# Optimization experiments

Measured on AMD Instinct MI355X. Metric: run time of the kernel, lower is better.

## Reference

```python
import jax, jax.numpy as jnp
import numpy as np

N = 100000   # nodes
E = 1600000  # edges
G = 512      # graphs
ATOM = 64
HID = 64
CLS = 10


def layer_norm(x, g, b, eps=1e-5):
    mu = jnp.mean(x, axis=-1, keepdims=True)
    var = jnp.mean((x - mu) ** 2, axis=-1, keepdims=True)
    return (x - mu) * jax.lax.rsqrt(var + eps) * g + b


def gcn_conv(x, src, dst, W, b, fill, num_nodes):
    # PyG GCNConv with add_self_loops: A_hat = A + fill*I, sym-normalized.
    h = x @ W                                            # [N, F_out]
    ones = jnp.ones(src.shape[0], dtype=h.dtype)
    deg = jax.ops.segment_sum(ones, dst, num_segments=num_nodes) + fill
    dinv = jax.lax.rsqrt(deg)                            # deg^{-1/2}
    norm = dinv[src] * dinv[dst]                         # [E]
    msg = h[src] * norm[:, None]                         # gather + scale
    out = jax.ops.segment_sum(msg, dst, num_segments=num_nodes)
    out = out + (fill * dinv * dinv)[:, None] * h        # self-loop term
    return out + b


def setup_inputs() -> dict:
    key = jax.random.key(0)
    ks = jax.random.split(key, 8)
    x = jax.random.normal(ks[0], (N, ATOM), dtype=jnp.float32)
    edge_index = jax.random.randint(ks[1], (2, E), 0, N, dtype=jnp.int64)
    batch = jnp.sort(jax.random.randint(ks[2], (N,), 0, G, dtype=jnp.int64))
    s = lambda k, sh, fan: jax.random.normal(k, sh, jnp.float32) / np.sqrt(fan)
    return {
        "x": x, "edge_index": edge_index, "batch": batch,
        "W1": s(ks[3], (ATOM, HID), ATOM), "b1": jnp.zeros((HID,), jnp.float32),
        "ln_g": jnp.ones((HID,), jnp.float32), "ln_b": jnp.zeros((HID,), jnp.float32),
        "W2": s(ks[4], (HID, HID), HID), "b2": jnp.zeros((HID,), jnp.float32),
        "W3": s(ks[5], (HID, 768), HID), "b3": jnp.zeros((768,), jnp.float32),
        "ln2_g": jnp.ones((768,), jnp.float32), "ln2_b": jnp.zeros((768,), jnp.float32),
        "W4": s(ks[6], (768, CLS), 768), "b4": jnp.zeros((CLS,), jnp.float32),
    }


def reference(x, edge_index, batch, W1, b1, ln_g, ln_b, W2, b2,
              W3, b3, ln2_g, ln2_b, W4, b4):
    src, dst = edge_index[0], edge_index[1]
    leaky = lambda v: jax.nn.leaky_relu(v, 0.2)
    # GCN1 (improved=True -> self-loop weight 2.0) + LN + LeakyReLU
    h = gcn_conv(x, src, dst, W1, b1, 2.0, N)
    h = leaky(layer_norm(h, ln_g, ln_b))
    # GCN2 (self-loop weight 1.0) + LeakyReLU
    h = gcn_conv(h, src, dst, W2, b2, 1.0, N)
    h = leaky(h)
    # global max pool over graphs
    pooled = jax.ops.segment_max(h, batch, num_segments=G)  # [G, HID]
    # seq2 head (Dropout is identity at inference)
    z = pooled @ W3 + b3
    z = leaky(layer_norm(z, ln2_g, ln2_b))
    z = z @ W4 + b4
    return jax.nn.softmax(z, axis=-1)
```

## Files before the change

### kernel.cpp

```cpp
#include <hip/hip_runtime.h>
#include <hip/hip_bf16.h>

#define NODES 100000
#define EDGES 1600000
#define NGRAPH 512
#define BINROWS 512
#define NBINS 196
#define BINCAP 12288
#define CHUNK 4096
#define NCHUNKS ((EDGES + CHUNK - 1) / CHUNK)
#define VSS 72
#define ZROW NODES

using bf16 = __hip_bfloat16;
typedef long long ll;
using frag8 = __attribute__((ext_vector_type(8))) short;
using f32x4 = __attribute__((ext_vector_type(4))) float;

__device__ __forceinline__ float lrelu(float v) { return v > 0.0f ? v : 0.2f * v; }

__device__ __forceinline__ unsigned mapf(float f) {
    unsigned u = __float_as_uint(f);
    return (u & 0x80000000u) ? ~u : (u | 0x80000000u);
}
__device__ __forceinline__ float unmapf(unsigned u) {
    return __uint_as_float((u & 0x80000000u) ? (u ^ 0x80000000u) : ~u);
}

__device__ __forceinline__ int idx_at(const void* raw, int i, int f) {
    return f ? (int)((const ll*)raw)[i] : ((const int*)raw)[i];
}

__device__ __forceinline__ unsigned short tobf(float f) {
    bf16 h = __float2bfloat16(f);
    return *reinterpret_cast<unsigned short*>(&h);
}

__global__ void sentinel_kernel(float* out, float v) {
    int i = blockIdx.x * blockDim.x + threadIdx.x;
    if (i < NGRAPH * 10) out[i] = v;
}

__global__ void binPlace(const int* __restrict__ eiw, int* __restrict__ flag,
                         int* __restrict__ binCursor, unsigned* __restrict__ staging) {
    __shared__ unsigned recs[CHUNK];
    __shared__ unsigned char binsA[CHUNK];
    __shared__ int hist[NBINS], lstart[NBINS + 1], baseg[NBINS], lcur[NBINS];
    __shared__ int red[4];
    int t = threadIdx.x;
    int e0 = blockIdx.x * CHUNK;
    int eEnd = min(e0 + CHUNK, EDGES);
    int v = 0;
    for (int k = e0 + t; k < eEnd; k += 256) v |= eiw[2 * k + 1];
    for (int o = 32; o; o >>= 1) v |= __shfl_xor(v, o);
    if ((t & 63) == 0) red[t >> 6] = v;
    if (t < NBINS) { hist[t] = 0; lcur[t] = 0; }
    __syncthreads();
    int f = ((red[0] | red[1] | red[2] | red[3]) == 0) ? 1 : 0;
    if (blockIdx.x == 0 && t == 0) flag[0] = f;
    const void* ei = (const void*)eiw;
    for (int i = e0 + t; i < eEnd; i += 256) {
        int s = idx_at(ei, i, f), d = idx_at(ei, EDGES + i, f);
        if ((unsigned)s < NODES && (unsigned)d < NODES) atomicAdd(&hist[d >> 9], 1);
    }
    __syncthreads();
    if (t == 0) {
        int acc = 0;
        for (int bb = 0; bb < NBINS; ++bb) {
            lstart[bb] = acc;
            acc += hist[bb];
        }
        lstart[NBINS] = acc;
    }
    __syncthreads();
    if (t < NBINS && hist[t] > 0) baseg[t] = atomicAdd(&binCursor[t], hist[t]);
    __syncthreads();
    for (int i = e0 + t; i < eEnd; i += 256) {
        int s = idx_at(ei, i, f), d = idx_at(ei, EDGES + i, f);
        if ((unsigned)s < NODES && (unsigned)d < NODES) {
            int bb = d >> 9;
            int p = lstart[bb] + atomicAdd(&lcur[bb], 1);
            recs[p] = ((unsigned)s << 9) | (unsigned)(d & 511);
            binsA[p] = (unsigned char)bb;
        }
    }
    __syncthreads();
    int nv = lstart[NBINS];
    for (int p = t; p < nv; p += 256) {
        int bb = binsA[p];
        int idx = baseg[bb] + (p - lstart[bb]);
        if (idx < BINCAP) staging[(size_t)bb * BINCAP + idx] = recs[p];
    }
}

__global__ void csr_finalize(const unsigned* __restrict__ staging,
                             const int* __restrict__ binCursor, int* __restrict__ row_ptr,
                             float* __restrict__ dinv1, float* __restrict__ dinv2,
                             int* __restrict__ csr_src) {
    __shared__ int lhist[BINROWS];
    __shared__ int sc[256];
    __shared__ int startSh;
    int b = blockIdx.x, t = threadIdx.x;
    int cv = (t < NBINS) ? binCursor[t] : 0;
    sc[t] = (t < b) ? cv : 0;
    __syncthreads();
    for (int o = 128; o; o >>= 1) {
        if (t < o) sc[t] += sc[t + o];
        __syncthreads();
    }
    if (t == 0) startSh = sc[0];
    __syncthreads();
    int myStart = startSh;
    int cnt = binCursor[b];
    if (b == NBINS - 1 && t == 0) row_ptr[NODES] = myStart + cnt;
    const unsigned* st = staging + (size_t)b * BINCAP;
    int r0 = b << 9;
    for (int j = t; j < BINROWS; j += 256) lhist[j] = 0;
    __syncthreads();
    for (int p = t; p < cnt; p += 256) atomicAdd(&lhist[st[p] & 511], 1);
    __syncthreads();
    int base = t * 2;
    int v0 = lhist[base], v1 = lhist[base + 1];
    int tsum = v0 + v1;
    sc[t] = tsum;
    __syncthreads();
    for (int o = 1; o < 256; o <<= 1) {
        int u = (t >= o) ? sc[t - o] : 0;
        __syncthreads();
        sc[t] += u;
        __syncthreads();
    }
    int excl = sc[t] - tsum;
    int ex0 = excl, ex1 = excl + v0;
#pragma unroll
    for (int k = 0; k < 2; ++k) {
        int row = r0 + base + k;
        int ex = k ? ex1 : ex0;
        int dgz = k ? v1 : v0;
        if (row < NODES) {
            row_ptr[row] = myStart + ex;
            float dg = (float)dgz;
            dinv1[row] = 1.0f / sqrtf(dg + 2.0f);
            dinv2[row] = 1.0f / sqrtf(dg + 1.0f);
        }
    }
    __syncthreads();
    lhist[base] = ex0;
    lhist[base + 1] = ex1;
    __syncthreads();
    for (int p = t; p < cnt; p += 256) {
        unsigned rec = st[p];
        int slot = atomicAdd(&lhist[rec & 511], 1);
        csr_src[myStart + slot] = (int)(rec >> 9);
    }
}

__global__ void prescale_x(const float* __restrict__ x, const float* __restrict__ dinv1,
                           bf16* __restrict__ xs, bf16* __restrict__ h1s) {
    int i = blockIdx.x * blockDim.x + threadIdx.x;
    if (i >= (NODES + 1) * 16) return;
    if (i >= NODES * 16) {
        uint2 z = make_uint2(0u, 0u);
        ((uint2*)xs)[i] = z;
        ((uint2*)h1s)[i] = z;
        return;
    }
    int row = i >> 4;
    float4 xv = ((const float4*)x)[i];
    float d1 = dinv1[row];
    uint2 p;
    p.x = (unsigned)tobf(xv.x * d1) | ((unsigned)tobf(xv.y * d1) << 16);
    p.y = (unsigned)tobf(xv.z * d1) | ((unsigned)tobf(xv.w * d1) << 16);
    ((uint2*)xs)[i] = p;
}

__device__ __forceinline__ void unpack_acc(uint2 u, float (&a)[4]) {
    a[0] += __uint_as_float(u.x << 16);
    a[1] += __uint_as_float(u.x & 0xffff0000u);
    a[2] += __uint_as_float(u.y << 16);
    a[3] += __uint_as_float(u.y & 0xffff0000u);
}

__device__ __forceinline__ void qreduce(float (&a)[4]) {
#pragma unroll
    for (int k = 0; k < 4; ++k) {
        a[k] += __shfl_xor(a[k], 16);
        a[k] += __shfl_xor(a[k], 32);
    }
}

__device__ __forceinline__ void finrow(const uint2* __restrict__ feat4,
                                       const float* __restrict__ dinv, float selfw,
                                       short* Vs, int rowBase, int rloc, int c,
                                       const float (&a)[4]) {
    int grow = rowBase + rloc;
    float dv = 0.0f;
    uint2 us = make_uint2(0u, 0u);
    if (grow < NODES) {
        dv = dinv[grow];
        us = feat4[(size_t)grow * 16 + c];
    }
    float v0 = dv * (a[0] + selfw * __uint_as_float(us.x << 16));
    float v1 = dv * (a[1] + selfw * __uint_as_float(us.x & 0xffff0000u));
    float v2 = dv * (a[2] + selfw * __uint_as_float(us.y << 16));
    float v3 = dv * (a[3] + selfw * __uint_as_float(us.y & 0xffff0000u));
    uint2 pk;
    pk.x = (unsigned)tobf(v0) | ((unsigned)tobf(v1) << 16);
    pk.y = (unsigned)tobf(v2) | ((unsigned)tobf(v3) << 16);
    *(uint2*)(Vs + (size_t)rloc * VSS + c * 4) = pk;
}

__device__ __forceinline__ void gcn_core(const uint2* __restrict__ feat4,
                                         const int* __restrict__ csr,
                                         const int* __restrict__ rp,
                                         const float* __restrict__ dinv, float selfw,
                                         const float* __restrict__ W, short* Vs, short* Wt,
                                         int rowBase, int lane, int wave, f32x4 (&acc)[4]) {
    int t = wave * 64 + lane;
    for (int i = t; i < 4096; i += 256) {
        int k = i >> 6, n = i & 63;
        Wt[n * VSS + k] = (short)tobf(W[i]);
    }
    __syncthreads();
    int myBase = rowBase + wave * 16;
    int rpv = (lane < 17) ? rp[min(myBase + lane, NODES)] : 0;
    int q = lane >> 4, c = lane & 15;
    for (int ii = 0; ii < 4; ++ii) {
        int iA = ii, iB = ii + 4, iC = ii + 8, iD = ii + 12;
        int cbA = __shfl(rpv, iA), endA = __shfl(rpv, iA + 1);
        int cbB = __shfl(rpv, iB), endB = __shfl(rpv, iB + 1);
        int cbC = __shfl(rpv, iC), endC = __shfl(rpv, iC + 1);
        int cbD = __shfl(rpv, iD), endD = __shfl(rpv, iD + 1);
        float aA[4] = {0, 0, 0, 0}, aB[4] = {0, 0, 0, 0};
        float aC[4] = {0, 0, 0, 0}, aD[4] = {0, 0, 0, 0};
        while (cbA < endA || cbB < endB || cbC < endC || cbD < endD) {
            int cntA = endA - cbA;
            cntA = cntA > 64 ? 64 : (cntA < 0 ? 0 : cntA);
            int cntB = endB - cbB;
            cntB = cntB > 64 ? 64 : (cntB < 0 ? 0 : cntB);
            int cntC = endC - cbC;
            cntC = cntC > 64 ? 64 : (cntC < 0 ? 0 : cntC);
            int cntD = endD - cbD;
            cntD = cntD > 64 ? 64 : (cntD < 0 ? 0 : cntD);
            int idxA = (lane < cntA) ? csr[cbA + lane] : 0;
            int idxB = (lane < cntB) ? csr[cbB + lane] : 0;
            int idxC = (lane < cntC) ? csr[cbC + lane] : 0;
            int idxD = (lane < cntD) ? csr[cbD + lane] : 0;
            int jm = max(max(cntA, cntB), max(cntC, cntD));
            for (int j = 0; j < jm; j += 8) {
                int e0 = j + q, e1 = j + 4 + q;
                int sA0 = __shfl(idxA, e0), sA1 = __shfl(idxA, e1);
                int sB0 = __shfl(idxB, e0), sB1 = __shfl(idxB, e1);
                int sC0 = __shfl(idxC, e0), sC1 = __shfl(idxC, e1);
                int sD0 = __shfl(idxD, e0), sD1 = __shfl(idxD, e1);
                sA0 = (e0 < cntA) ? sA0 : ZROW;
                sA1 = (e1 < cntA) ? sA1 : ZROW;
                sB0 = (e0 < cntB) ? sB0 : ZROW;
                sB1 = (e1 < cntB) ? sB1 : ZROW;
                sC0 = (e0 < cntC) ? sC0 : ZROW;
                sC1 = (e1 < cntC) ? sC1 : ZROW;
                sD0 = (e0 < cntD) ? sD0 : ZROW;
                sD1 = (e1 < cntD) ? sD1 : ZROW;
                uint2 uA0 = feat4[(size_t)sA0 * 16 + c];
                uint2 uA1 = feat4[(size_t)sA1 * 16 + c];
                uint2 uB0 = feat4[(size_t)sB0 * 16 + c];
                uint2 uB1 = feat4[(size_t)sB1 * 16 + c];
                uint2 uC0 = feat4[(size_t)sC0 * 16 + c];
                uint2 uC1 = feat4[(size_t)sC1 * 16 + c];
                uint2 uD0 = feat4[(size_t)sD0 * 16 + c];
                uint2 uD1 = feat4[(size_t)sD1 * 16 + c];
                unpack_acc(uA0, aA);
                unpack_acc(uA1, aA);
                unpack_acc(uB0, aB);
                unpack_acc(uB1, aB);
                unpack_acc(uC0, aC);
                unpack_acc(uC1, aC);
                unpack_acc(uD0, aD);
                unpack_acc(uD1, aD);
            }
            cbA += 64;
            cbB += 64;
            cbC += 64;
            cbD += 64;
        }
        qreduce(aA);
        qreduce(aB);
        qreduce(aC);
        qreduce(aD);
        if (lane < 16) {
            finrow(feat4, dinv, selfw, Vs, rowBase, wave * 16 + iA, c, aA);
            finrow(feat4, dinv, selfw, Vs, rowBase, wave * 16 + iB, c, aB);
            finrow(feat4, dinv, selfw, Vs, rowBase, wave * 16 + iC, c, aC);
            finrow(feat4, dinv, selfw, Vs, rowBase, wave * 16 + iD, c, aD);
        }
    }
    frag8 afr[2];
    int m = lane & 15;
#pragma unroll
    for (int ks = 0; ks < 2; ++ks)
        afr[ks] = *(frag8*)(Vs + (size_t)(wave * 16 + m) * VSS + q * 8 + ks * 32);
#pragma unroll
    for (int nt = 0; nt < 4; ++nt) {
        f32x4 a = {0.f, 0.f, 0.f, 0.f};
#pragma unroll
        for (int ks = 0; ks < 2; ++ks) {
            frag8 bfr = *(frag8*)(Wt + (size_t)(nt * 16 + m) * VSS + q * 8 + ks * 32);
            a = __builtin_amdgcn_mfma_f32_16x16x32_bf16(afr[ks], bfr, a, 0, 0, 0);
        }
        acc[nt] = a;
    }
}

__global__ void __launch_bounds__(256, 2)
gcn1_fused(const uint2* __restrict__ xs4, const int* __restrict__ csr,
           const int* __restrict__ rp, const float* __restrict__ dinv1,
           const float* __restrict__ dinv2, const float* __restrict__ W1,
           const float* __restrict__ b1, const float* __restrict__ lng,
           const float* __restrict__ lnb, bf16* __restrict__ h1s) {
    __shared__ short sm[2 * 64 * VSS];
    short* Vs = sm;
    short* Wt = sm + 64 * VSS;
    int lane = threadIdx.x & 63, wave = threadIdx.x >> 6;
    int rowBase = blockIdx.x * 64;
    f32x4 acc[4];
    gcn_core(xs4, csr, rp, dinv1, 2.0f, W1, Vs, Wt, rowBase, lane, wave, acc);
    int c = lane & 15, q = lane >> 4;
    float bc[4], lg[4], lb[4];
#pragma unroll
    for (int nt = 0; nt < 4; ++nt) {
        bc[nt] = b1[nt * 16 + c];
        lg[nt] = lng[nt * 16 + c];
        lb[nt] = lnb[nt * 16 + c];
    }
#pragma unroll
    for (int r = 0; r < 4; ++r) {
        int grow = rowBase + wave * 16 + q * 4 + r;
        float v0 = acc[0][r] + bc[0], v1 = acc[1][r] + bc[1];
        float v2 = acc[2][r] + bc[2], v3 = acc[3][r] + bc[3];
        float s = v0 + v1 + v2 + v3;
        for (int o = 1; o < 16; o <<= 1) s += __shfl_xor(s, o);
        float mu = s * (1.0f / 64.0f);
        float d0 = v0 - mu, d1 = v1 - mu, d2 = v2 - mu, d3 = v3 - mu;
        float qq = d0 * d0 + d1 * d1 + d2 * d2 + d3 * d3;
        for (int o = 1; o < 16; o <<= 1) qq += __shfl_xor(qq, o);
        float rstd = 1.0f / sqrtf(qq * (1.0f / 64.0f) + 1e-5f);
        if (grow < NODES) {
            float d2v = dinv2[grow];
            bf16* dst = h1s + (size_t)grow * 64 + c;
            dst[0]  = __float2bfloat16(lrelu(d0 * rstd * lg[0] + lb[0]) * d2v);
            dst[16] = __float2bfloat16(lrelu(d1 * rstd * lg[1] + lb[1]) * d2v);
            dst[32] = __float2bfloat16(lrelu(d2 * rstd * lg[2] + lb[2]) * d2v);
            dst[48] = __float2bfloat16(lrelu(d3 * rstd * lg[3] + lb[3]) * d2v);
        }
    }
}

__global__ void __launch_bounds__(256, 2)
gcn2_fused(const uint2* __restrict__ h1s4, const int* __restrict__ csr,
           const int* __restrict__ rp, const float* __restrict__ dinv2,
           const float* __restrict__ W2, const float* __restrict__ b2,
           const void* __restrict__ batch, const int* __restrict__ flag,
           unsigned* __restrict__ pooled) {
    __shared__ short sm[2 * 64 * VSS];
    __shared__ int gsh[64];
    short* Vs = sm;
    short* Wt = sm + 64 * VSS;
    int t = threadIdx.x, lane = t & 63, wave = t >> 6;
    int rowBase = blockIdx.x * 64;
    if (t < 64) {
        int row = rowBase + t;
        gsh[t] = (row < NODES) ? idx_at(batch, row, flag[0]) : -1;
    }
    f32x4 acc[4];
    gcn_core(h1s4, csr, rp, dinv2, 1.0f, W2, Vs, Wt, rowBase, lane, wave, acc);
    int c = lane & 15, q = lane >> 4;
    float bc[4];
#pragma unroll
    for (int nt = 0; nt < 4; ++nt) bc[nt] = b2[nt * 16 + c];
    __syncthreads();
    float* P = (float*)sm;
#pragma unroll
    for (int r = 0; r < 4; ++r) {
        int mloc = wave * 16 + q * 4 + r;
#pragma unroll
        for (int nt = 0; nt < 4; ++nt)
            P[(size_t)mloc * 65 + nt * 16 + c] = lrelu(acc[nt][r] + bc[nt]);
    }
    __syncthreads();
    if (wave == 0) {
        float m = P[lane];
        int gc = gsh[0];
        for (int r = 1; r < 64; ++r) {
            int gr = gsh[r];
            float ar = P[(size_t)r * 65 + lane];
            if (gr == gc) {
                m = fmaxf(m, ar);
            } else {
                if ((unsigned)gc < NGRAPH) atomicMax(&pooled[gc * 64 + lane], mapf(m));
                gc = gr;
                m = ar;
            }
        }
        if ((unsigned)gc < NGRAPH) atomicMax(&pooled[gc * 64 + lane], mapf(m));
    }
}

__global__ void head_kernel(const unsigned* __restrict__ pooled, const float* __restrict__ W3,
                            const float* __restrict__ b3, const float* __restrict__ g2,
                            const float* __restrict__ be2, const float* __restrict__ W4,
                            const float* __restrict__ b4, float* __restrict__ out) {
    __shared__ float prow[64];
    __shared__ float z[768];
    __shared__ float rs[4], rss[4];
    __shared__ float mu_s, rstd_s;
    __shared__ float red[10];
    int t = threadIdx.x, gI = blockIdx.x;
    if (t < 64) prow[t] = unmapf(pooled[gI * 64 + t]);
    __syncthreads();
    for (int c = t; c < 768; c += 256) {
        float acc = b3[c];
#pragma unroll 16
        for (int k = 0; k < 64; ++k) acc += prow[k] * W3[k * 768 + c];
        z[c] = acc;
    }
    __syncthreads();
    float s = 0.0f, ss = 0.0f;
    for (int c = t; c < 768; c += 256) {
        float v = z[c];
        s += v;
        ss += v * v;
    }
    for (int o = 32; o; o >>= 1) {
        s += __shfl_xor(s, o);
        ss += __shfl_xor(ss, o);
    }
    if ((t & 63) == 0) { rs[t >> 6] = s; rss[t >> 6] = ss; }
    __syncthreads();
    if (t == 0) {
        float S = rs[0] + rs[1] + rs[2] + rs[3];
        float SS = rss[0] + rss[1] + rss[2] + rss[3];
        float mu = S * (1.0f / 768.0f);
        float var = SS * (1.0f / 768.0f) - mu * mu;
        mu_s = mu;
        rstd_s = 1.0f / sqrtf(fmaxf(var, 0.0f) + 1e-5f);
    }
    __syncthreads();
    for (int c = t; c < 768; c += 256) {
        float y = (z[c] - mu_s) * rstd_s * g2[c] + be2[c];
        z[c] = lrelu(y);
    }
    if (t < 10) red[t] = 0.0f;
    __syncthreads();
    float p[10];
#pragma unroll
    for (int c = 0; c < 10; ++c) p[c] = 0.0f;
    for (int k = t; k < 768; k += 256) {
        float zv = z[k];
#pragma unroll
        for (int c = 0; c < 10; ++c) p[c] += zv * W4[k * 10 + c];
    }
#pragma unroll
    for (int c = 0; c < 10; ++c) atomicAdd(&red[c], p[c]);
    __syncthreads();
    if (t == 0) {
        float l[10], m = -1e30f;
#pragma unroll
        for (int c = 0; c < 10; ++c) {
            l[c] = red[c] + b4[c];
            m = fmaxf(m, l[c]);
        }
        float sum = 0.0f;
#pragma unroll
        for (int c = 0; c < 10; ++c) {
            l[c] = expf(l[c] - m);
            sum += l[c];
        }
        float inv = 1.0f / sum;
#pragma unroll
        for (int c = 0; c < 10; ++c) out[gI * 10 + c] = l[c] * inv;
    }
}

extern "C" void kernel_launch(void* const* d_in, const int* in_sizes, int n_in,
                              void* d_out, int out_size, void* d_ws, size_t ws_size,
                              hipStream_t stream) {
    const size_t REQUIRED = (size_t)(NODES + 1) * 64 * 2 * 2
                          + (size_t)EDGES * 4
                          + (size_t)(NODES + 1) * 4
                          + (size_t)NODES * 4 * 2
                          + (size_t)NBINS * 4
                          + (size_t)NGRAPH * 64 * 4
                          + 16;
    if (ws_size < REQUIRED) {
        sentinel_kernel<<<20, 256, 0, stream>>>((float*)d_out, 64.0f);
        return;
    }

    const float* x = (const float*)d_in[0];
    const int* eiw = (const int*)d_in[1];
    const void* batch = d_in[2];
    const float* W1 = (const float*)d_in[3];
    const float* b1 = (const float*)d_in[4];
    const float* lng = (const float*)d_in[5];
    const float* lnb = (const float*)d_in[6];
    const float* W2 = (const float*)d_in[7];
    const float* b2 = (const float*)d_in[8];
    const float* W3 = (const float*)d_in[9];
    const float* b3 = (const float*)d_in[10];
    const float* g2 = (const float*)d_in[11];
    const float* be2 = (const float*)d_in[12];
    const float* W4 = (const float*)d_in[13];
    const float* b4 = (const float*)d_in[14];

    bf16* xs = (bf16*)d_ws;
    bf16* h1s = xs + (size_t)(NODES + 1) * 64;
    unsigned* staging = (unsigned*)h1s;
    int* csr_src = (int*)(h1s + (size_t)(NODES + 1) * 64);
    int* row_ptr = csr_src + EDGES;
    float* dinv1 = (float*)(row_ptr + NODES + 1);
    float* dinv2 = dinv1 + NODES;
    int* binCursor = (int*)(dinv2 + NODES);
    unsigned* pooled = (unsigned*)(binCursor + NBINS);
    int* flag = (int*)(pooled + NGRAPH * 64);

    hipMemsetAsync(binCursor, 0, (size_t)NBINS * 4, stream);
    hipMemsetAsync(pooled, 0, (size_t)NGRAPH * 64 * 4, stream);

    binPlace<<<NCHUNKS, 256, 0, stream>>>(eiw, flag, binCursor, staging);
    csr_finalize<<<NBINS, 256, 0, stream>>>(staging, binCursor, row_ptr, dinv1, dinv2,
                                            csr_src);
    prescale_x<<<((NODES + 1) * 16 + 255) / 256, 256, 0, stream>>>(x, dinv1, xs, h1s);

    gcn1_fused<<<(NODES + 63) / 64, 256, 0, stream>>>((const uint2*)xs, csr_src, row_ptr,
                                                      dinv1, dinv2, W1, b1, lng, lnb, h1s);
    gcn2_fused<<<(NODES + 63) / 64, 256, 0, stream>>>((const uint2*)h1s, csr_src, row_ptr,
                                                      dinv2, W2, b2, batch, flag, pooled);

    head_kernel<<<NGRAPH, 256, 0, stream>>>(pooled, W3, b3, g2, be2, W4, b4, (float*)d_out);
}
```

Baseline: 290.4 us.

## Halve CSR bin width and chunk size, parallelize bin prefix scan

Buckets destinations into 256-row bins (391 bins) and processes edges in 2048-edge chunks, so binPlace and csr_finalize launch roughly twice as many blocks, and each csr_finalize thread handles one row. The serial single-thread prefix over bins in binPlace becomes a parallel Hillis-Steele scan, and the two memsets are merged into one. The aim is better occupancy and less serial work in CSR construction. In exchange there are more global atomics on binCursor and a smaller per-bin capacity that could overflow if degrees are skewed.

```diff
diff --git a/kernel.cpp b/kernel.cpp
--- a/kernel.cpp
+++ b/kernel.cpp
@@ -4,10 +4,10 @@
 #define NODES 100000
 #define EDGES 1600000
 #define NGRAPH 512
-#define BINROWS 512
-#define NBINS 196
-#define BINCAP 12288
-#define CHUNK 4096
+#define BINROWS 256
+#define NBINS 391
+#define BINCAP 6144
+#define CHUNK 2048
 #define NCHUNKS ((EDGES + CHUNK - 1) / CHUNK)
 #define VSS 72
 #define ZROW NODES
@@ -44,8 +44,9 @@
 __global__ void binPlace(const int* __restrict__ eiw, int* __restrict__ flag,
                          int* __restrict__ binCursor, unsigned* __restrict__ staging) {
     __shared__ unsigned recs[CHUNK];
-    __shared__ unsigned char binsA[CHUNK];
+    __shared__ unsigned short binsA[CHUNK];
     __shared__ int hist[NBINS], lstart[NBINS + 1], baseg[NBINS], lcur[NBINS];
+    __shared__ int sc[256];
     __shared__ int red[4];
     int t = threadIdx.x;
     int e0 = blockIdx.x * CHUNK;
@@ -54,34 +55,43 @@
     for (int k = e0 + t; k < eEnd; k += 256) v |= eiw[2 * k + 1];
     for (int o = 32; o; o >>= 1) v |= __shfl_xor(v, o);
     if ((t & 63) == 0) red[t >> 6] = v;
-    if (t < NBINS) { hist[t] = 0; lcur[t] = 0; }
+    for (int j = t; j < NBINS; j += 256) { hist[j] = 0; lcur[j] = 0; }
     __syncthreads();
     int f = ((red[0] | red[1] | red[2] | red[3]) == 0) ? 1 : 0;
     if (blockIdx.x == 0 && t == 0) flag[0] = f;
     const void* ei = (const void*)eiw;
     for (int i = e0 + t; i < eEnd; i += 256) {
         int s = idx_at(ei, i, f), d = idx_at(ei, EDGES + i, f);
-        if ((unsigned)s < NODES && (unsigned)d < NODES) atomicAdd(&hist[d >> 9], 1);
-    }
-    __syncthreads();
-    if (t == 0) {
-        int acc = 0;
-        for (int bb = 0; bb < NBINS; ++bb) {
-            lstart[bb] = acc;
-            acc += hist[bb];
-        }
-        lstart[NBINS] = acc;
-    }
-    __syncthreads();
-    if (t < NBINS && hist[t] > 0) baseg[t] = atomicAdd(&binCursor[t], hist[t]);
+        if ((unsigned)s < NODES && (unsigned)d < NODES) atomicAdd(&hist[d >> 8], 1);
+    }
+    __syncthreads();
+    int b0 = t * 2, b1 = t * 2 + 1;
+    int h0 = (b0 < NBINS) ? hist[b0] : 0;
+    int h1 = (b1 < NBINS) ? hist[b1] : 0;
+    int ts = h0 + h1;
+    sc[t] = ts;
+    __syncthreads();
+    for (int o = 1; o < 256; o <<= 1) {
+        int u = (t >= o) ? sc[t - o] : 0;
+        __syncthreads();
+        sc[t] += u;
+        __syncthreads();
+    }
+    int excl = sc[t] - ts;
+    if (b0 < NBINS) lstart[b0] = excl;
+    if (b1 < NBINS) lstart[b1] = excl + h0;
+    if (t == 255) lstart[NBINS] = sc[255];
+    __syncthreads();
+    for (int j = t; j < NBINS; j += 256)
+        if (hist[j] > 0) baseg[j] = atomicAdd(&binCursor[j], hist[j]);
     __syncthreads();
     for (int i = e0 + t; i < eEnd; i += 256) {
         int s = idx_at(ei, i, f), d = idx_at(ei, EDGES + i, f);
         if ((unsigned)s < NODES && (unsigned)d < NODES) {
-            int bb = d >> 9;
+            int bb = d >> 8;
             int p = lstart[bb] + atomicAdd(&lcur[bb], 1);
-            recs[p] = ((unsigned)s << 9) | (unsigned)(d & 511);
-            binsA[p] = (unsigned char)bb;
+            recs[p] = ((unsigned)s << 8) | (unsigned)(d & 255);
+            binsA[p] = (unsigned short)bb;
         }
     }
     __syncthreads();
@@ -101,8 +111,10 @@
     __shared__ int sc[256];
     __shared__ int startSh;
     int b = blockIdx.x, t = threadIdx.x;
-    int cv = (t < NBINS) ? binCursor[t] : 0;
-    sc[t] = (t < b) ? cv : 0;
+    int b0 = t * 2, b1 = t * 2 + 1;
+    int c0 = (b0 < NBINS) ? binCursor[b0] : 0;
+    int c1 = (b1 < NBINS) ? binCursor[b1] : 0;
+    sc[t] = ((b0 < b) ? c0 : 0) + ((b1 < b) ? c1 : 0);
     __syncthreads();
     for (int o = 128; o; o >>= 1) {
         if (t < o) sc[t] += sc[t + o];
@@ -114,15 +126,13 @@
     int cnt = binCursor[b];
     if (b == NBINS - 1 && t == 0) row_ptr[NODES] = myStart + cnt;
     const unsigned* st = staging + (size_t)b * BINCAP;
-    int r0 = b << 9;
-    for (int j = t; j < BINROWS; j += 256) lhist[j] = 0;
-    __syncthreads();
-    for (int p = t; p < cnt; p += 256) atomicAdd(&lhist[st[p] & 511], 1);
-    __syncthreads();
-    int base = t * 2;
-    int v0 = lhist[base], v1 = lhist[base + 1];
-    int tsum = v0 + v1;
-    sc[t] = tsum;
+    int r0 = b << 8;
+    lhist[t] = 0;
+    __syncthreads();
+    for (int p = t; p < cnt; p += 256) atomicAdd(&lhist[st[p] & 255], 1);
+    __syncthreads();
+    int dg = lhist[t];
+    sc[t] = dg;
     __syncthreads();
     for (int o = 1; o < 256; o <<= 1) {
         int u = (t >= o) ? sc[t - o] : 0;
@@ -130,28 +140,21 @@
         sc[t] += u;
         __syncthreads();
     }
-    int excl = sc[t] - tsum;
-    int ex0 = excl, ex1 = excl + v0;
-#pragma unroll
-    for (int k = 0; k < 2; ++k) {
-        int row = r0 + base + k;
-        int ex = k ? ex1 : ex0;
-        int dgz = k ? v1 : v0;
-        if (row < NODES) {
-            row_ptr[row] = myStart + ex;
-            float dg = (float)dgz;
-            dinv1[row] = 1.0f / sqrtf(dg + 2.0f);
-            dinv2[row] = 1.0f / sqrtf(dg + 1.0f);
-        }
-    }
-    __syncthreads();
-    lhist[base] = ex0;
-    lhist[base + 1] = ex1;
+    int excl = sc[t] - dg;
+    int row = r0 + t;
+    if (row < NODES) {
+        row_ptr[row] = myStart + excl;
+        float dgf = (float)dg;
+        dinv1[row] = 1.0f / sqrtf(dgf + 2.0f);
+        dinv2[row] = 1.0f / sqrtf(dgf + 1.0f);
+    }
+    __syncthreads();
+    lhist[t] = excl;
     __syncthreads();
     for (int p = t; p < cnt; p += 256) {
         unsigned rec = st[p];
-        int slot = atomicAdd(&lhist[rec & 511], 1);
-        csr_src[myStart + slot] = (int)(rec >> 9);
+        int slot = atomicAdd(&lhist[rec & 255], 1);
+        csr_src[myStart + slot] = (int)(rec >> 8);
     }
 }
 
@@ -523,8 +526,7 @@
     unsigned* pooled = (unsigned*)(binCursor + NBINS);
     int* flag = (int*)(pooled + NGRAPH * 64);
 
-    hipMemsetAsync(binCursor, 0, (size_t)NBINS * 4, stream);
-    hipMemsetAsync(pooled, 0, (size_t)NGRAPH * 64 * 4, stream);
+    hipMemsetAsync(binCursor, 0, ((size_t)NBINS + (size_t)NGRAPH * 64) * 4, stream);
 
     binPlace<<<NCHUNKS, 256, 0, stream>>>(eiw, flag, binCursor, staging);
     csr_finalize<<<NBINS, 256, 0, stream>>>(staging, binCursor, row_ptr, dinv1, dinv2,
```

After: 282.6 us. 1.03x faster.
